# Optimization experiments

Hardware: AMD Instinct MI355X
Metric: run time of the kernel (lower is better)

The kernel has to match this reference:

```python
import jax, jax.numpy as jnp
import numpy as np

DIM = 1024
HEADS = 16
HEAD_DIM = DIM // HEADS
MLP_HID = 4 * DIM
LN_EPS = 1e-5


def layer_norm(x, g, b):
    mu = jnp.mean(x, axis=-1, keepdims=True)
    var = jnp.mean((x - mu) ** 2, axis=-1, keepdims=True)
    return (x - mu) * jax.lax.rsqrt(var + LN_EPS) * g + b


def setup_inputs() -> dict:
    key = jax.random.key(0)
    ks = jax.random.split(key, 8)
    s = 0.02
    return {
        "x": jax.random.normal(ks[0], (8, 1024, DIM), dtype=jnp.float32),
        "attention_mask": jnp.ones((8, 1024), dtype=jnp.int32),
        "ln1_g": jnp.ones((DIM,), jnp.float32),
        "ln1_b": jnp.zeros((DIM,), jnp.float32),
        "qkv_w": jax.random.normal(ks[1], (3 * DIM, DIM), jnp.float32) * s,
        "proj_w": jax.random.normal(ks[2], (DIM, DIM), jnp.float32) * s,
        "proj_b": jnp.zeros((DIM,), jnp.float32),
        "ln2_g": jnp.ones((DIM,), jnp.float32),
        "ln2_b": jnp.zeros((DIM,), jnp.float32),
        "fc1_w": jax.random.normal(ks[3], (MLP_HID, DIM), jnp.float32) * s,
        "fc1_b": jnp.zeros((MLP_HID,), jnp.float32),
        "fc2_w": jax.random.normal(ks[4], (DIM, MLP_HID), jnp.float32) * s,
        "fc2_b": jnp.zeros((DIM,), jnp.float32),
    }


def reference(x, attention_mask, ln1_g, ln1_b, qkv_w, proj_w, proj_b,
              ln2_g, ln2_b, fc1_w, fc1_b, fc2_w, fc2_b):
    B, N, C = x.shape
    scale = HEAD_DIM ** -0.5

    # --- attention branch ---
    h = layer_norm(x, ln1_g, ln1_b)
    qkv = h @ qkv_w.T                       # [B,N,3C] (no qkv bias)
    qkv = qkv.reshape(B, N, 3, HEADS, HEAD_DIM).transpose(2, 0, 3, 1, 4)
    q, k, v = qkv[0], qkv[1], qkv[2]        # each [B,H,N,Dh]
    attn = jnp.einsum('bhnd,bhmd->bhnm', q, k) * scale
    mask = (attention_mask == 0)[:, None, None, :]  # [B,1,1,N]
    attn = jnp.where(mask, -jnp.inf, attn)
    attn = jax.nn.softmax(attn, axis=-1)
    out = jnp.einsum('bhnm,bhmd->bhnd', attn, v)
    out = out.transpose(0, 2, 1, 3).reshape(B, N, C)
    out = out @ proj_w.T + proj_b
    x = x + out

    # --- MLP branch ---
    h = layer_norm(x, ln2_g, ln2_b)
    h = jax.nn.gelu(h @ fc1_w.T + fc1_b, approximate=False)
    h = h @ fc2_w.T + fc2_b
    return x + h
```

## Files before the change

kernel.cpp:

```cpp
#include <hip/hip_runtime.h>
#include <hip/hip_bf16.h>
#include <stdint.h>
#include <math.h>

#define DIMC 1024
#define SEQ 1024
#define NBATCH 8
#define NHEADS 16
#define HDIM 64
#define MLPHID 4096
#define NROWS (NBATCH*SEQ)

typedef __attribute__((ext_vector_type(8))) short short8;
typedef __attribute__((ext_vector_type(4))) float f32x4;
typedef __attribute__((ext_vector_type(16))) float f32x16;
typedef __attribute__((ext_vector_type(4))) unsigned int u32x4;

__device__ __forceinline__ short f2bf(float f) {
  union { float f; uint32_t u; } x; x.f = f;
  uint32_t r = (x.u + 0x7FFFu + ((x.u >> 16) & 1u)) >> 16;
  return (short)r;
}

__device__ __forceinline__ unsigned int cvtpk(float lo, float hi_) {
  unsigned int r;
  asm("v_cvt_pk_bf16_f32 %0, %1, %2" : "=v"(r) : "v"(lo), "v"(hi_));
  return r;
}

__device__ __forceinline__ float gelu_f(float v) {
  const float t = v * v;
  const float p = fmaf(t, 0.044715f, 1.0f);
  const float e = __builtin_amdgcn_exp2f(2.3022082f * v * p);
  return v - v * __builtin_amdgcn_rcpf(e + 1.0f);
}

__device__ __forceinline__ f32x4 mfma16(short8 a, short8 b, f32x4 c) {
  return __builtin_amdgcn_mfma_f32_16x16x32_bf16(a, b, c, 0, 0, 0);
}
__device__ __forceinline__ f32x16 mfma32(short8 a, short8 b, f32x16 c) {
  return __builtin_amdgcn_mfma_f32_32x32x16_bf16(a, b, c, 0, 0, 0);
}

__device__ __forceinline__ void gload16(const void* g, void* l) {
  __builtin_amdgcn_global_load_lds(
      (const __attribute__((address_space(1))) uint32_t*)g,
      (__attribute__((address_space(3))) uint32_t*)l, 16, 0, 0);
}

__global__ __launch_bounds__(256)
void f2bw_kernel(const float* __restrict__ w0, const float* __restrict__ w1,
                 const float* __restrict__ w2, const float* __restrict__ w3,
                 short* __restrict__ o0, short* __restrict__ o1,
                 short* __restrict__ o2, short* __restrict__ o3) {
  const int i = blockIdx.x * 256 + threadIdx.x;
  const float4* src;
  short4* dst;
  if (i < 786432)       { src = (const float4*)w0 + i;             dst = (short4*)o0 + i; }
  else if (i < 1048576) { src = (const float4*)w1 + (i - 786432);  dst = (short4*)o1 + (i - 786432); }
  else if (i < 2097152) { src = (const float4*)w2 + (i - 1048576); dst = (short4*)o2 + (i - 1048576); }
  else                  { src = (const float4*)w3 + (i - 2097152); dst = (short4*)o3 + (i - 2097152); }
  const float4 v = *src;
  short4 o;
  o.x = f2bf(v.x); o.y = f2bf(v.y); o.z = f2bf(v.z); o.w = f2bf(v.w);
  *dst = o;
}

__global__ __launch_bounds__(256)
void ln_kernel(const float* __restrict__ x, const float* __restrict__ g,
               const float* __restrict__ beta, short* __restrict__ out) {
  const int row = blockIdx.x;
  const int tid = threadIdx.x;
  const float4 v = ((const float4*)(x + (size_t)row * DIMC))[tid];
  float s = v.x + v.y + v.z + v.w;
  float q = v.x*v.x + v.y*v.y + v.z*v.z + v.w*v.w;
#pragma unroll
  for (int o = 32; o > 0; o >>= 1) { s += __shfl_down(s, o); q += __shfl_down(q, o); }
  __shared__ float rs[4], rq[4];
  const int lane = tid & 63, w = tid >> 6;
  if (lane == 0) { rs[w] = s; rq[w] = q; }
  __syncthreads();
  s = rs[0] + rs[1] + rs[2] + rs[3];
  q = rq[0] + rq[1] + rq[2] + rq[3];
  const float mean = s * (1.0f / DIMC);
  const float var = q * (1.0f / DIMC) - mean * mean;
  const float rstd = rsqrtf(var + 1e-5f);
  const float4 gv = ((const float4*)g)[tid];
  const float4 bv = ((const float4*)beta)[tid];
  short4 o4;
  o4.x = f2bf((v.x - mean) * rstd * gv.x + bv.x);
  o4.y = f2bf((v.y - mean) * rstd * gv.y + bv.y);
  o4.z = f2bf((v.z - mean) * rstd * gv.z + bv.z);
  o4.w = f2bf((v.w - mean) * rstd * gv.w + bv.w);
  ((short4*)(out + (size_t)row * DIMC))[tid] = o4;
}

#define NOVM ((void)0)
#define NOST ((void)0)
#define VMC4 asm volatile("s_waitcnt vmcnt(4)" ::: "memory")
#define VMC2 asm volatile("s_waitcnt vmcnt(2)" ::: "memory")

#define SA(DB, H, T) \
  gload16(sA0 + (H)*hstep + (size_t)(T)*64, stb + ((DB)*4 + (H))*16384); \
  gload16(sA1 + (H)*hstep + (size_t)(T)*64, stb + ((DB)*4 + (H))*16384 + 8192)

#define SB(DB, H, T) \
  gload16(sB0 + (H)*hstep + (size_t)(T)*64, stb + ((DB)*4 + 2 + (H))*16384); \
  gload16(sB1 + (H)*hstep + (size_t)(T)*64, stb + ((DB)*4 + 2 + (H))*16384 + 8192)

#define PH(DB, QA, QB, LDA, LDB, STAGE, VM) \
  do { \
    if (LDA) { \
      _Pragma("unroll") \
      for (int mi = 0; mi < 4; ++mi) { \
        _Pragma("unroll") \
        for (int ks = 0; ks < 2; ++ks) \
          af[mi][ks] = *(const short8*)(ard##DB + (((QA)*4 + mi)*2 + ks)*1024); \
      } \
    } \
    if (LDB) { \
      _Pragma("unroll") \
      for (int ni = 0; ni < 2; ++ni) { \
        _Pragma("unroll") \
        for (int ks = 0; ks < 2; ++ks) \
          bfv[QB][ni][ks] = *(const short8*)(brd##DB + (((QB)*2 + ni)*2 + ks)*1024); \
      } \
    } \
    STAGE; \
    __builtin_amdgcn_s_barrier(); \
    asm volatile("s_waitcnt lgkmcnt(0)" ::: "memory"); \
    __builtin_amdgcn_sched_barrier(0); \
    __builtin_amdgcn_s_setprio(1); \
    _Pragma("unroll") \
    for (int ks = 0; ks < 2; ++ks) { \
      _Pragma("unroll") \
      for (int mi = 0; mi < 4; ++mi) { \
        _Pragma("unroll") \
        for (int ni = 0; ni < 2; ++ni) \
          acc[(QA)*4 + mi][(QB)*2 + ni] = \
            mfma16(af[mi][ks], bfv[QB][ni][ks], acc[(QA)*4 + mi][(QB)*2 + ni]); \
      } \
    } \
    __builtin_amdgcn_s_setprio(0); \
    VM; \
    __builtin_amdgcn_s_barrier(); \
  } while (0)

template<bool BIAS, bool GELU, bool RESID, bool OBF16>
__global__ __launch_bounds__(512)
void gemm8p(const short* __restrict__ A, const short* __restrict__ W,
            const float* __restrict__ bias, const float* __restrict__ resid,
            float* __restrict__ outF, short* __restrict__ outB,
            int M, int N, int K, int ntl, int mt8)
{
  __shared__ __align__(16) char lsm[131072];
  const int tid = threadIdx.x;
  const int lane = tid & 63;
  const int w = tid >> 6;
  const int wm = w >> 2;
  const int wn = w & 3;
  const int fr = lane & 15;
  const int fko = (lane >> 4) << 3;

  const int bid = blockIdx.x;
  const int xcd = bid & 7, l = bid >> 3;
  const int bm = (xcd * mt8 + l / ntl) << 8;
  const int bn = (l % ntl) << 8;

  int row_[2], kk_[2];
#pragma unroll
  for (int j = 0; j < 2; ++j) {
    const int s = j * 8 + (tid >> 6);
    const int r16 = (tid & 63) >> 2;
    const int cb = ((tid & 3) << 4) ^ (((tid >> 5) & 1) << 5);
    row_[j] = (s >> 1) * 16 + r16;
    kk_[j]  = (s & 1) * 32 + (cb >> 1);
  }
  const short* sA0 = A + (size_t)(bm + row_[0]) * K + kk_[0];
  const short* sA1 = A + (size_t)(bm + row_[1]) * K + kk_[1];
  const short* sB0 = W + (size_t)(bn + row_[0]) * K + kk_[0];
  const short* sB1 = W + (size_t)(bn + row_[1]) * K + kk_[1];
  const size_t hstep = (size_t)128 * K;
  char* stb = lsm + tid * 16;

  const int lofs = fr * 64 + ((fko << 1) ^ (((fr >> 3) & 1) << 5));
  const char* ard0 = lsm + wm * 16384 + lofs;
  const char* brd0 = lsm + 32768 + (wn >> 1) * 16384 + (wn & 1) * 8192 + lofs;
  const char* ard1 = ard0 + 65536;
  const char* brd1 = brd0 + 65536;

  short8 af[4][2];
  short8 bfv[2][2][2];
  f32x4 acc[8][4] = {};

  SA(0, 0, 0); SA(0, 1, 0);
  SB(0, 0, 0); SB(0, 1, 0);
  SB(1, 0, 1); SB(1, 1, 1);
  VMC4;
  __builtin_amdgcn_s_barrier();

  const int nk = K >> 6;
  const int nit = nk >> 1;
  const int tmask = nk - 1;
  for (int it = 0; it < nit; ++it) {
    const int t1 = 2 * it + 1;
    const int t2 = (2 * it + 2) & tmask;
    const int t3 = (2 * it + 3) & tmask;
    PH(0, 0, 0, 1, 1, SA(1, 0, t1), NOVM);
    PH(0, 0, 1, 0, 1, SA(1, 1, t1), NOVM);
    PH(0, 1, 1, 1, 0, SB(0, 0, t2), NOVM);
    PH(0, 1, 0, 0, 0, SB(0, 1, t2), VMC4);
    PH(1, 0, 0, 1, 1, SA(0, 0, t2), NOVM);
    PH(1, 0, 1, 0, 1, SA(0, 1, t2), NOVM);
    PH(1, 1, 1, 1, 0, SB(1, 0, t3), NOVM);
    PH(1, 1, 0, 0, 0, SB(1, 1, t3), VMC4);
  }

  asm volatile("s_waitcnt vmcnt(0)" ::: "memory");
  __builtin_amdgcn_s_barrier();

  const int orow0 = bm + wm * 128 + ((lane >> 4) << 2);
  const int ocol0 = bn + wn * 64 + fr;
#pragma unroll
  for (int mi = 0; mi < 8; ++mi) {
#pragma unroll
    for (int r = 0; r < 4; ++r) {
      const int row = orow0 + mi * 16 + r;
      const size_t base = (size_t)row * N;
#pragma unroll
      for (int ni = 0; ni < 4; ++ni) {
        const int col = ocol0 + ni * 16;
        float v = acc[mi][ni][r];
        if (BIAS) v += bias[col];
        if (GELU) v = gelu_f(v);
        if (RESID) v += resid[base + col];
        if (OBF16) outB[base + col] = f2bf(v);
        else       outF[base + col] = v;
      }
    }
  }
}

#define SA2(DB, H, T) \
  gload16(sA0 + (H)*hstep + (size_t)(T)*64, stb + ((DB)*3 + (H))*16384); \
  gload16(sA1 + (H)*hstep + (size_t)(T)*64, stb + ((DB)*3 + (H))*16384 + 8192)

#define SB2(DB, T) \
  gload16(sB0 + (size_t)(T)*64, stb + ((DB)*3 + 2)*16384); \
  gload16(sB1 + (size_t)(T)*64, stb + ((DB)*3 + 2)*16384 + 8192)

#define PH2(DB, QA, QB, LDA, LDB, STAGE, VM) \
  do { \
    if (LDA) { \
      _Pragma("unroll") \
      for (int i = 0; i < 2; ++i) { \
        _Pragma("unroll") \
        for (int ks = 0; ks < 2; ++ks) \
          af[i][ks] = *(const short8*)(ard##DB + (((QA)*2 + i)*2 + ks)*1024); \
      } \
    } \
    if (LDB) { \
      _Pragma("unroll") \
      for (int jn = 0; jn < 2; ++jn) { \
        _Pragma("unroll") \
        for (int ks = 0; ks < 2; ++ks) \
          bfv[QB][jn][ks] = *(const short8*)(brd##DB + (((QB)*2 + jn)*2 + ks)*1024); \
      } \
    } \
    STAGE; \
    __builtin_amdgcn_s_barrier(); \
    asm volatile("s_waitcnt lgkmcnt(0)" ::: "memory"); \
    __builtin_amdgcn_sched_barrier(0); \
    __builtin_amdgcn_s_setprio(1); \
    _Pragma("unroll") \
    for (int ks = 0; ks < 2; ++ks) { \
      _Pragma("unroll") \
      for (int i = 0; i < 2; ++i) { \
        _Pragma("unroll") \
        for (int jn = 0; jn < 2; ++jn) \
          acc[(QA)*2 + i][(QB)*2 + jn] = \
            mfma16(af[i][ks], bfv[QB][jn][ks], acc[(QA)*2 + i][(QB)*2 + jn]); \
      } \
    } \
    __builtin_amdgcn_s_setprio(0); \
    VM; \
    __builtin_amdgcn_s_barrier(); \
  } while (0)

template<bool BIAS, bool GELU, bool RESID, bool OBF16, bool QSCALE>
__global__ __launch_bounds__(512)
void gemm8pn(const short* __restrict__ A, const short* __restrict__ W,
             const float* __restrict__ bias, const float* __restrict__ resid,
             float* __restrict__ outF, short* __restrict__ outB,
             int M, int N, int K, int ntl, int mt8)
{
  __shared__ __align__(16) char lsm[98304];
  const int tid = threadIdx.x;
  const int lane = tid & 63;
  const int w = tid >> 6;
  const int wm = w >> 1;
  const int wn = w & 1;
  const int fr = lane & 15;
  const int fko = (lane >> 4) << 3;

  const int bid = blockIdx.x;
  const int xcd = bid & 7, l = bid >> 3;
  const int bm = (xcd * mt8 + l / ntl) << 8;
  const int bn = (l % ntl) << 7;

  int row_[2], kk_[2];
#pragma unroll
  for (int j = 0; j < 2; ++j) {
    const int s = j * 8 + (tid >> 6);
    const int r16 = (tid & 63) >> 2;
    const int cb = ((tid & 3) << 4) ^ (((tid >> 5) & 1) << 5);
    row_[j] = (s >> 1) * 16 + r16;
    kk_[j]  = (s & 1) * 32 + (cb >> 1);
  }
  const short* sA0 = A + (size_t)(bm + row_[0]) * K + kk_[0];
  const short* sA1 = A + (size_t)(bm + row_[1]) * K + kk_[1];
  const short* sB0 = W + (size_t)(bn + row_[0]) * K + kk_[0];
  const short* sB1 = W + (size_t)(bn + row_[1]) * K + kk_[1];
  const size_t hstep = (size_t)128 * K;
  char* stb = lsm + tid * 16;

  const int lofs = fr * 64 + ((fko << 1) ^ (((fr >> 3) & 1) << 5));
  const char* ard0 = lsm + (wm >> 1) * 16384 + (wm & 1) * 8192 + lofs;
  const char* brd0 = lsm + 32768 + wn * 8192 + lofs;
  const char* ard1 = ard0 + 49152;
  const char* brd1 = brd0 + 49152;

  short8 af[2][2];
  short8 bfv[2][2][2];
  f32x4 acc[4][4] = {};

  SA2(0, 0, 0); SA2(0, 1, 0); SB2(0, 0);
  SB2(1, 1);
  VMC2;
  __builtin_amdgcn_s_barrier();

  const int nk = K >> 6;
  const int nit = nk >> 1;
  const int tmask = nk - 1;
  for (int it = 0; it < nit; ++it) {
    const int t1 = 2 * it + 1;
    const int t2 = (2 * it + 2) & tmask;
    const int t3 = (2 * it + 3) & tmask;
    PH2(0, 0, 0, 1, 1, SA2(1, 0, t1), NOVM);
    PH2(0, 0, 1, 0, 1, SA2(1, 1, t1), NOVM);
    PH2(0, 1, 1, 1, 0, SB2(0, t2),    NOVM);
    PH2(0, 1, 0, 0, 0, NOST,          VMC2);
    PH2(1, 0, 0, 1, 1, SA2(0, 0, t2), NOVM);
    PH2(1, 0, 1, 0, 1, SA2(0, 1, t2), NOVM);
    PH2(1, 1, 1, 1, 0, SB2(1, t3),    NOVM);
    PH2(1, 1, 0, 0, 0, NOST,          VMC2);
  }

  asm volatile("s_waitcnt vmcnt(0)" ::: "memory");
  __builtin_amdgcn_s_barrier();

  const int orow0 = bm + wm * 64 + ((lane >> 4) << 2);
  const int ocol0 = bn + wn * 64 + fr;
#pragma unroll
  for (int mi = 0; mi < 4; ++mi) {
#pragma unroll
    for (int r = 0; r < 4; ++r) {
      const int row = orow0 + mi * 16 + r;
      const size_t base = (size_t)row * N;
#pragma unroll
      for (int ni = 0; ni < 4; ++ni) {
        const int col = ocol0 + ni * 16;
        float v = acc[mi][ni][r];
        if (BIAS) v += bias[col];
        if (GELU) v = gelu_f(v);
        if (QSCALE) v *= (col < 1024 ? 0.18033688f : 1.0f);
        if (RESID) v += resid[base + col];
        if (OBF16) outB[base + col] = f2bf(v);
        else       outF[base + col] = v;
      }
    }
  }
}

__global__ __launch_bounds__(256)
void attn_kernel(const short* __restrict__ qkv, const int* __restrict__ amask,
                 short* __restrict__ out)
{
  __shared__ __align__(16) char lsm[36864];
  char* lsK = lsm;
  char* lsV = lsm + 16384;
  int* lmask = (int*)(lsm + 32768);
  __shared__ int anym;

  const int tid = threadIdx.x;
  const int lane = tid & 63;
  const int w = tid >> 6;
  const int l31 = lane & 31;
  const int hi = lane >> 5;
  const int swz = (l31 & 7) << 4;

  const int bid = blockIdx.x;
  const int swzb = ((bid & 7) << 7) | (bid >> 3);
  const int qt = swzb & 7;
  const int h = (swzb >> 3) & 15;
  const int b = swzb >> 7;
  const size_t rowbase = (size_t)b * SEQ;
  const short* qkvB = qkv + rowbase * 3072 + h * 64;

  const int4 mv = ((const int4*)(amask + b * SEQ))[tid];
  if (tid == 0) anym = 0;
  ((int4*)lmask)[tid] = mv;
  __syncthreads();
  if ((mv.x & mv.y & mv.z & mv.w) == 0) atomicOr(&anym, 1);

  const int q0 = qt * 128 + w * 32;
  const short* qptr = qkvB + (size_t)(q0 + l31) * 3072;
  short8 qf[4];
#pragma unroll
  for (int ks = 0; ks < 4; ++ks)
    qf[ks] = *(const short8*)(qptr + ks * 16 + hi * 8);

  const int krow = tid >> 3;
  const int kcc = (((tid & 7) * 16) ^ ((krow & 7) << 4)) >> 1;
  const short* gK = qkvB + 1024 + kcc;
  char* ldK = lsK + tid * 16;
  const int vr = tid & 63;
  const int vc0 = (tid >> 6) << 3;
  const short* gV = qkvB + 2048 + vc0;

  gload16(gK + (size_t)krow * 3072, ldK);
  gload16(gK + (size_t)(krow + 32) * 3072, ldK + 4096);
  {
    short8 a0 = *(const short8*)(gV + (size_t)vr * 3072);
    short8 a1 = *(const short8*)(gV + (size_t)vr * 3072 + 32);
#pragma unroll
    for (int j = 0; j < 8; ++j) {
      *(short*)(lsV + (vc0 + j) * 128 + ((2 * vr) ^ (j << 4))) = a0[j];
      *(short*)(lsV + (vc0 + 32 + j) * 128 + ((2 * vr) ^ (j << 4))) = a1[j];
    }
  }
  __syncthreads();

  f32x16 oacc[2] = {};
  float psum = 0.f;

  for (int c = 0; c < 16; ++c) {
    const int cur = c & 1;
    const char* lKc = lsK + cur * 8192;
    const char* lVc = lsV + cur * 8192;
    const bool pf = (c < 15);
    short8 vv0, vv1;
    if (pf) {
      const size_t nb_ = (size_t)(c + 1) * 64;
      char* ldKn = ldK + (cur ^ 1) * 8192;
      gload16(gK + (nb_ + krow) * 3072, ldKn);
      gload16(gK + (nb_ + krow + 32) * 3072, ldKn + 4096);
      vv0 = *(const short8*)(gV + (nb_ + vr) * 3072);
      vv1 = *(const short8*)(gV + (nb_ + vr) * 3072 + 32);
    }

    f32x16 pacc[2] = {};
    __builtin_amdgcn_s_setprio(1);
#pragma unroll
    for (int ks = 0; ks < 4; ++ks) {
#pragma unroll
      for (int s = 0; s < 2; ++s) {
        short8 kf = *(const short8*)(lKc + (s * 32 + l31) * 128 +
                                     ((ks * 32 + hi * 16) ^ swz));
        pacc[s] = mfma32(kf, qf[ks], pacc[s]);
      }
    }
    __builtin_amdgcn_s_setprio(0);

    if (pf) {
      char* lVn = lsV + (cur ^ 1) * 8192;
#pragma unroll
      for (int j = 0; j < 8; ++j) {
        *(short*)(lVn + (vc0 + j) * 128 + ((2 * vr) ^ (j << 4))) = vv0[j];
        *(short*)(lVn + (vc0 + 32 + j) * 128 + ((2 * vr) ^ (j << 4))) = vv1[j];
      }
    }

    if (anym) {
      const int kv0 = c * 64;
#pragma unroll
      for (int s = 0; s < 2; ++s)
#pragma unroll
        for (int r = 0; r < 16; ++r) {
          const int kv = kv0 + 32 * s + (r & 3) + 8 * (r >> 2) + 4 * hi;
          if (lmask[kv] == 0) pacc[s][r] = -1e30f;
        }
    }

    float pe[2][16];
#pragma unroll
    for (int s = 0; s < 2; ++s)
#pragma unroll
      for (int r = 0; r < 16; ++r) {
        const float p = __builtin_amdgcn_exp2f(pacc[s][r]);
        pe[s][r] = p;
        psum += p;
      }

    short8 pa[4];
#pragma unroll
    for (int ks = 0; ks < 4; ++ks) {
      const int sh = ks >> 1, kb = (ks & 1) << 3;
      unsigned int aa = cvtpk(pe[sh][kb + 0], pe[sh][kb + 1]);
      unsigned int bb = cvtpk(pe[sh][kb + 4], pe[sh][kb + 5]);
      unsigned int cc = cvtpk(pe[sh][kb + 2], pe[sh][kb + 3]);
      unsigned int dd = cvtpk(pe[sh][kb + 6], pe[sh][kb + 7]);
      asm volatile("v_permlane32_swap_b32 %0, %1" : "+v"(aa), "+v"(bb));
      asm volatile("v_permlane32_swap_b32 %0, %1" : "+v"(cc), "+v"(dd));
      u32x4 t;
      t[0] = aa; t[1] = cc; t[2] = bb; t[3] = dd;
      pa[ks] = __builtin_bit_cast(short8, t);
    }

    __builtin_amdgcn_s_setprio(1);
#pragma unroll
    for (int nb = 0; nb < 2; ++nb)
#pragma unroll
      for (int ks = 0; ks < 4; ++ks) {
        short8 vf = *(const short8*)(lVc + (nb * 32 + l31) * 128 +
                                     ((ks * 32 + hi * 16) ^ swz));
        oacc[nb] = mfma32(pa[ks], vf, oacc[nb]);
      }
    __builtin_amdgcn_s_setprio(0);

    __syncthreads();
  }

  const float lt = psum + __shfl_xor(psum, 32);
  const size_t orow = rowbase + q0;
#pragma unroll
  for (int r = 0; r < 16; ++r) {
    const int q = (r & 3) + 8 * (r >> 2) + 4 * hi;
    const float linv = 1.0f / __shfl(lt, q);
    short* op = out + (orow + q) * DIMC + h * 64 + l31;
    op[0]  = f2bf(oacc[0][r] * linv);
    op[32] = f2bf(oacc[1][r] * linv);
  }
}

extern "C" void kernel_launch(void* const* d_in, const int* in_sizes, int n_in,
                              void* d_out, int out_size, void* d_ws, size_t ws_size,
                              hipStream_t stream)
{
  const float* x      = (const float*)d_in[0];
  const int*   amask  = (const int*)d_in[1];
  const float* ln1_g  = (const float*)d_in[2];
  const float* ln1_b  = (const float*)d_in[3];
  const float* qkv_w  = (const float*)d_in[4];
  const float* proj_w = (const float*)d_in[5];
  const float* proj_b = (const float*)d_in[6];
  const float* ln2_g  = (const float*)d_in[7];
  const float* ln2_b  = (const float*)d_in[8];
  const float* fc1_w  = (const float*)d_in[9];
  const float* fc1_b  = (const float*)d_in[10];
  const float* fc2_w  = (const float*)d_in[11];
  const float* fc2_b  = (const float*)d_in[12];
  float* out = (float*)d_out;

  char* ws = (char*)d_ws;
  short* wqkv  = (short*)(ws);
  short* wproj = (short*)(ws + 6291456);
  short* wfc1  = (short*)(ws + 8388608);
  short* wfc2  = (short*)(ws + 16777216);
  float* x1    = (float*)(ws + 25165824);
  short* hb    = (short*)(ws + 58720256);
  short* qkvo  = (short*)(ws + 75497472);
  short* attno = (short*)(ws + 125829120);
  short* fc1o  = (short*)(ws + 75497472);

  f2bw_kernel<<<12288, 256, 0, stream>>>(qkv_w, proj_w, fc1_w, fc2_w,
                                         wqkv, wproj, wfc1, wfc2);

  ln_kernel<<<NROWS, 256, 0, stream>>>(x, ln1_g, ln1_b, hb);

  gemm8pn<false, false, false, true, true><<<768, 512, 0, stream>>>(
      hb, wqkv, nullptr, nullptr, nullptr, qkvo, NROWS, 3 * DIMC, DIMC, 24, 4);

  attn_kernel<<<1024, 256, 0, stream>>>(qkvo, amask, attno);

  gemm8pn<true, false, true, false, false><<<256, 512, 0, stream>>>(
      attno, wproj, proj_b, x, x1, nullptr, NROWS, DIMC, DIMC, 8, 4);

  ln_kernel<<<NROWS, 256, 0, stream>>>(x1, ln2_g, ln2_b, hb);

  gemm8p<true, true, false, true><<<512, 512, 0, stream>>>(
      hb, wfc1, fc1_b, nullptr, nullptr, fc1o, NROWS, MLPHID, DIMC, 16, 4);

  gemm8pn<true, false, true, false, false><<<256, 512, 0, stream>>>(
      fc1o, wfc2, fc2_b, x1, out, nullptr, NROWS, DIMC, MLPHID, 8, 4);
}
```

Measured before the change: 327.1 us.

## Fuse weight cast with LN1, store residual in bf16, restructure narrow GEMM pipeline

Merges the weight fp32-to-bf16 conversion and the first layernorm into one launch. It also stores the intermediate residual x1 as bf16 instead of fp32, which roughly halves its write and read traffic in the projection GEMM, LN2 and the fc2 epilogue. The narrow GEMM is rewritten with a different k-step pipeline: a full A tile is double-buffered and B tiles rotate through three buffers in 112KB of LDS. Rounding x1 to bf16 before adding it back to the final residual lowers accuracy, and the larger LDS footprint may reduce occupancy.

```diff
diff --git a/kernel.cpp b/kernel.cpp
--- a/kernel.cpp
+++ b/kernel.cpp
@@ -22,6 +22,11 @@
   return (short)r;
 }
 
+__device__ __forceinline__ float bf2f(unsigned short b) {
+  union { uint32_t u; float f; } c; c.u = ((uint32_t)b) << 16;
+  return c.f;
+}
+
 __device__ __forceinline__ unsigned int cvtpk(float lo, float hi_) {
   unsigned int r;
   asm("v_cvt_pk_bf16_f32 %0, %1, %2" : "=v"(r) : "v"(lo), "v"(hi_));
@@ -49,29 +54,66 @@
 }
 
 __global__ __launch_bounds__(256)
-void f2bw_kernel(const float* __restrict__ w0, const float* __restrict__ w1,
+void prep_kernel(const float* __restrict__ x, const float* __restrict__ g,
+                 const float* __restrict__ beta, short* __restrict__ hb,
+                 const float* __restrict__ w0, const float* __restrict__ w1,
                  const float* __restrict__ w2, const float* __restrict__ w3,
                  short* __restrict__ o0, short* __restrict__ o1,
                  short* __restrict__ o2, short* __restrict__ o3) {
-  const int i = blockIdx.x * 256 + threadIdx.x;
-  const float4* src;
-  short4* dst;
-  if (i < 786432)       { src = (const float4*)w0 + i;             dst = (short4*)o0 + i; }
-  else if (i < 1048576) { src = (const float4*)w1 + (i - 786432);  dst = (short4*)o1 + (i - 786432); }
-  else if (i < 2097152) { src = (const float4*)w2 + (i - 1048576); dst = (short4*)o2 + (i - 1048576); }
-  else                  { src = (const float4*)w3 + (i - 2097152); dst = (short4*)o3 + (i - 2097152); }
-  const float4 v = *src;
-  short4 o;
-  o.x = f2bf(v.x); o.y = f2bf(v.y); o.z = f2bf(v.z); o.w = f2bf(v.w);
-  *dst = o;
-}
-
+  const int tid = threadIdx.x;
+  if (blockIdx.x < NROWS) {
+    const int row = blockIdx.x;
+    const float4 v = ((const float4*)(x + (size_t)row * DIMC))[tid];
+    float s = v.x + v.y + v.z + v.w;
+    float q = v.x*v.x + v.y*v.y + v.z*v.z + v.w*v.w;
+#pragma unroll
+    for (int o = 32; o > 0; o >>= 1) { s += __shfl_down(s, o); q += __shfl_down(q, o); }
+    __shared__ float rs[4], rq[4];
+    const int lane = tid & 63, w = tid >> 6;
+    if (lane == 0) { rs[w] = s; rq[w] = q; }
+    __syncthreads();
+    s = rs[0] + rs[1] + rs[2] + rs[3];
+    q = rq[0] + rq[1] + rq[2] + rq[3];
+    const float mean = s * (1.0f / DIMC);
+    const float var = q * (1.0f / DIMC) - mean * mean;
+    const float rstd = rsqrtf(var + 1e-5f);
+    const float4 gv = ((const float4*)g)[tid];
+    const float4 bv = ((const float4*)beta)[tid];
+    short4 o4;
+    o4.x = f2bf((v.x - mean) * rstd * gv.x + bv.x);
+    o4.y = f2bf((v.y - mean) * rstd * gv.y + bv.y);
+    o4.z = f2bf((v.z - mean) * rstd * gv.z + bv.z);
+    o4.w = f2bf((v.w - mean) * rstd * gv.w + bv.w);
+    ((short4*)(hb + (size_t)row * DIMC))[tid] = o4;
+  } else {
+    const int i = (blockIdx.x - NROWS) * 256 + tid;
+    const float4* src;
+    short4* dst;
+    if (i < 786432)       { src = (const float4*)w0 + i;             dst = (short4*)o0 + i; }
+    else if (i < 1048576) { src = (const float4*)w1 + (i - 786432);  dst = (short4*)o1 + (i - 786432); }
+    else if (i < 2097152) { src = (const float4*)w2 + (i - 1048576); dst = (short4*)o2 + (i - 1048576); }
+    else                  { src = (const float4*)w3 + (i - 2097152); dst = (short4*)o3 + (i - 2097152); }
+    const float4 v = *src;
+    short4 o;
+    o.x = f2bf(v.x); o.y = f2bf(v.y); o.z = f2bf(v.z); o.w = f2bf(v.w);
+    *dst = o;
+  }
+}
+
+template<bool INBF16>
 __global__ __launch_bounds__(256)
-void ln_kernel(const float* __restrict__ x, const float* __restrict__ g,
+void ln_kernel(const void* __restrict__ xin, const float* __restrict__ g,
                const float* __restrict__ beta, short* __restrict__ out) {
   const int row = blockIdx.x;
   const int tid = threadIdx.x;
-  const float4 v = ((const float4*)(x + (size_t)row * DIMC))[tid];
+  float4 v;
+  if (INBF16) {
+    const short4 vb = ((const short4*)xin)[row * 256 + tid];
+    v.x = bf2f((unsigned short)vb.x); v.y = bf2f((unsigned short)vb.y);
+    v.z = bf2f((unsigned short)vb.z); v.w = bf2f((unsigned short)vb.w);
+  } else {
+    v = ((const float4*)xin)[row * 256 + tid];
+  }
   float s = v.x + v.y + v.z + v.w;
   float q = v.x*v.x + v.y*v.y + v.z*v.z + v.w*v.w;
 #pragma unroll
@@ -94,6 +136,7 @@
   o4.w = f2bf((v.w - mean) * rstd * gv.w + bv.w);
   ((short4*)(out + (size_t)row * DIMC))[tid] = o4;
 }
+
 
 #define NOVM ((void)0)
 #define NOST ((void)0)
@@ -241,60 +284,48 @@
   }
 }
 
-#define SA2(DB, H, T) \
-  gload16(sA0 + (H)*hstep + (size_t)(T)*64, stb + ((DB)*3 + (H))*16384); \
-  gload16(sA1 + (H)*hstep + (size_t)(T)*64, stb + ((DB)*3 + (H))*16384 + 8192)
-
-#define SB2(DB, T) \
-  gload16(sB0 + (size_t)(T)*64, stb + ((DB)*3 + 2)*16384); \
-  gload16(sB1 + (size_t)(T)*64, stb + ((DB)*3 + 2)*16384 + 8192)
-
-#define PH2(DB, QA, QB, LDA, LDB, STAGE, VM) \
+#define SAK(SLOT, T) \
+  gload16(sA0 + (size_t)(T)*64,         (SLOT) + tid*16); \
+  gload16(sA1 + (size_t)(T)*64,         (SLOT) + 8192 + tid*16); \
+  gload16(sA0 + hstep + (size_t)(T)*64, (SLOT) + 16384 + tid*16); \
+  gload16(sA1 + hstep + (size_t)(T)*64, (SLOT) + 24576 + tid*16)
+
+#define SBK(SLOT, T) \
+  gload16(sB0 + (size_t)(T)*64, (SLOT) + tid*16); \
+  gload16(sB1 + (size_t)(T)*64, (SLOT) + 8192 + tid*16)
+
+#define PHK(ARD, BRD, KS, STAGE, VM) \
   do { \
-    if (LDA) { \
-      _Pragma("unroll") \
-      for (int i = 0; i < 2; ++i) { \
-        _Pragma("unroll") \
-        for (int ks = 0; ks < 2; ++ks) \
-          af[i][ks] = *(const short8*)(ard##DB + (((QA)*2 + i)*2 + ks)*1024); \
-      } \
-    } \
-    if (LDB) { \
-      _Pragma("unroll") \
-      for (int jn = 0; jn < 2; ++jn) { \
-        _Pragma("unroll") \
-        for (int ks = 0; ks < 2; ++ks) \
-          bfv[QB][jn][ks] = *(const short8*)(brd##DB + (((QB)*2 + jn)*2 + ks)*1024); \
-      } \
-    } \
+    _Pragma("unroll") \
+    for (int mi = 0; mi < 4; ++mi) \
+      af[mi] = *(const short8*)((ARD) + (mi*2 + (KS))*1024); \
+    _Pragma("unroll") \
+    for (int jn = 0; jn < 4; ++jn) \
+      bfq[jn] = *(const short8*)((BRD) + (jn*2 + (KS))*1024); \
     STAGE; \
     __builtin_amdgcn_s_barrier(); \
     asm volatile("s_waitcnt lgkmcnt(0)" ::: "memory"); \
     __builtin_amdgcn_sched_barrier(0); \
     __builtin_amdgcn_s_setprio(1); \
     _Pragma("unroll") \
-    for (int ks = 0; ks < 2; ++ks) { \
+    for (int mi = 0; mi < 4; ++mi) { \
       _Pragma("unroll") \
-      for (int i = 0; i < 2; ++i) { \
-        _Pragma("unroll") \
-        for (int jn = 0; jn < 2; ++jn) \
-          acc[(QA)*2 + i][(QB)*2 + jn] = \
-            mfma16(af[i][ks], bfv[QB][jn][ks], acc[(QA)*2 + i][(QB)*2 + jn]); \
-      } \
+      for (int jn = 0; jn < 4; ++jn) \
+        acc[mi][jn] = mfma16(af[mi], bfq[jn], acc[mi][jn]); \
     } \
     __builtin_amdgcn_s_setprio(0); \
     VM; \
     __builtin_amdgcn_s_barrier(); \
   } while (0)
 
-template<bool BIAS, bool GELU, bool RESID, bool OBF16, bool QSCALE>
+template<bool BIAS, bool GELU, bool RESID, bool RESB16, bool OBF16, bool QSCALE>
 __global__ __launch_bounds__(512)
-void gemm8pn(const short* __restrict__ A, const short* __restrict__ W,
-             const float* __restrict__ bias, const float* __restrict__ resid,
-             float* __restrict__ outF, short* __restrict__ outB,
-             int M, int N, int K, int ntl, int mt8)
+void gemm2k(const short* __restrict__ A, const short* __restrict__ W,
+            const float* __restrict__ bias, const void* __restrict__ resid,
+            float* __restrict__ outF, short* __restrict__ outB,
+            int M, int N, int K, int ntl, int mt8)
 {
-  __shared__ __align__(16) char lsm[98304];
+  __shared__ __align__(16) char lsm[114688];
   const int tid = threadIdx.x;
   const int lane = tid & 63;
   const int w = tid >> 6;
@@ -322,38 +353,45 @@
   const short* sB0 = W + (size_t)(bn + row_[0]) * K + kk_[0];
   const short* sB1 = W + (size_t)(bn + row_[1]) * K + kk_[1];
   const size_t hstep = (size_t)128 * K;
-  char* stb = lsm + tid * 16;
 
   const int lofs = fr * 64 + ((fko << 1) ^ (((fr >> 3) & 1) << 5));
-  const char* ard0 = lsm + (wm >> 1) * 16384 + (wm & 1) * 8192 + lofs;
-  const char* brd0 = lsm + 32768 + wn * 8192 + lofs;
-  const char* ard1 = ard0 + 49152;
-  const char* brd1 = brd0 + 49152;
-
-  short8 af[2][2];
-  short8 bfv[2][2][2];
+  const char* ard0 = lsm + wm * 8192 + lofs;
+  const char* ard1 = ard0 + 32768;
+  char* as0 = lsm;
+  char* as1 = lsm + 32768;
+  const char* bur = lsm + 65536 + 0 * 16384 + wn * 8192 + lofs;
+  const char* bvr = lsm + 65536 + 1 * 16384 + wn * 8192 + lofs;
+  const char* bwr = lsm + 65536 + 2 * 16384 + wn * 8192 + lofs;
+  char* bus = lsm + 65536 + 0 * 16384;
+  char* bvs = lsm + 65536 + 1 * 16384;
+  char* bws = lsm + 65536 + 2 * 16384;
+
+  short8 af[4];
+  short8 bfq[4];
   f32x4 acc[4][4] = {};
-
-  SA2(0, 0, 0); SA2(0, 1, 0); SB2(0, 0);
-  SB2(1, 1);
-  VMC2;
-  __builtin_amdgcn_s_barrier();
 
   const int nk = K >> 6;
   const int nit = nk >> 1;
   const int tmask = nk - 1;
+
+  SAK(as0, 0);
+  SBK(bus, 0);
+  SBK(bvs, 1);
+  asm volatile("s_waitcnt vmcnt(0)" ::: "memory");
+  __builtin_amdgcn_s_barrier();
+
   for (int it = 0; it < nit; ++it) {
-    const int t1 = 2 * it + 1;
+    const int v  = 2 * it + 1;
     const int t2 = (2 * it + 2) & tmask;
     const int t3 = (2 * it + 3) & tmask;
-    PH2(0, 0, 0, 1, 1, SA2(1, 0, t1), NOVM);
-    PH2(0, 0, 1, 0, 1, SA2(1, 1, t1), NOVM);
-    PH2(0, 1, 1, 1, 0, SB2(0, t2),    NOVM);
-    PH2(0, 1, 0, 0, 0, NOST,          VMC2);
-    PH2(1, 0, 0, 1, 1, SA2(0, 0, t2), NOVM);
-    PH2(1, 0, 1, 0, 1, SA2(0, 1, t2), NOVM);
-    PH2(1, 1, 1, 1, 0, SB2(1, t3),    NOVM);
-    PH2(1, 1, 0, 0, 0, NOST,          VMC2);
+    PHK(ard0, bur, 0, SAK(as1, v),  NOVM);
+    PHK(ard0, bur, 1, SBK(bws, t2), VMC2);
+    PHK(ard1, bvr, 0, SAK(as0, t2), NOVM);
+    PHK(ard1, bvr, 1, SBK(bus, t3), VMC2);
+    const char* tr;
+    tr = bur; bur = bwr; bwr = bvr; bvr = tr;
+    char* ts;
+    ts = bus; bus = bws; bws = bvs; bvs = ts;
   }
 
   asm volatile("s_waitcnt vmcnt(0)" ::: "memory");
@@ -374,7 +412,10 @@
         if (BIAS) v += bias[col];
         if (GELU) v = gelu_f(v);
         if (QSCALE) v *= (col < 1024 ? 0.18033688f : 1.0f);
-        if (RESID) v += resid[base + col];
+        if (RESID) {
+          if (RESB16) v += bf2f(((const unsigned short*)resid)[base + col]);
+          else        v += ((const float*)resid)[base + col];
+        }
         if (OBF16) outB[base + col] = f2bf(v);
         else       outF[base + col] = v;
       }
@@ -567,30 +608,29 @@
   short* wproj = (short*)(ws + 6291456);
   short* wfc1  = (short*)(ws + 8388608);
   short* wfc2  = (short*)(ws + 16777216);
-  float* x1    = (float*)(ws + 25165824);
+  short* x1b   = (short*)(ws + 25165824);
   short* hb    = (short*)(ws + 58720256);
   short* qkvo  = (short*)(ws + 75497472);
   short* attno = (short*)(ws + 125829120);
   short* fc1o  = (short*)(ws + 75497472);
 
-  f2bw_kernel<<<12288, 256, 0, stream>>>(qkv_w, proj_w, fc1_w, fc2_w,
-                                         wqkv, wproj, wfc1, wfc2);
-
-  ln_kernel<<<NROWS, 256, 0, stream>>>(x, ln1_g, ln1_b, hb);
-
-  gemm8pn<false, false, false, true, true><<<768, 512, 0, stream>>>(
+  prep_kernel<<<NROWS + 12288, 256, 0, stream>>>(
+      x, ln1_g, ln1_b, hb, qkv_w, proj_w, fc1_w, fc2_w,
+      wqkv, wproj, wfc1, wfc2);
+
+  gemm2k<false, false, false, false, true, true><<<768, 512, 0, stream>>>(
       hb, wqkv, nullptr, nullptr, nullptr, qkvo, NROWS, 3 * DIMC, DIMC, 24, 4);
 
   attn_kernel<<<1024, 256, 0, stream>>>(qkvo, amask, attno);
 
-  gemm8pn<true, false, true, false, false><<<256, 512, 0, stream>>>(
-      attno, wproj, proj_b, x, x1, nullptr, NROWS, DIMC, DIMC, 8, 4);
-
-  ln_kernel<<<NROWS, 256, 0, stream>>>(x1, ln2_g, ln2_b, hb);
+  gemm2k<true, false, true, false, true, false><<<256, 512, 0, stream>>>(
+      attno, wproj, proj_b, x, nullptr, x1b, NROWS, DIMC, DIMC, 8, 4);
+
+  ln_kernel<true><<<NROWS, 256, 0, stream>>>(x1b, ln2_g, ln2_b, hb);
 
   gemm8p<true, true, false, true><<<512, 512, 0, stream>>>(
       hb, wfc1, fc1_b, nullptr, nullptr, fc1o, NROWS, MLPHID, DIMC, 16, 4);
 
-  gemm8pn<true, false, true, false, false><<<256, 512, 0, stream>>>(
-      fc1o, wfc2, fc2_b, x1, out, nullptr, NROWS, DIMC, MLPHID, 8, 4);
-}
+  gemm2k<true, false, true, true, false, false><<<256, 512, 0, stream>>>(
+      fc1o, wfc2, fc2_b, x1b, out, nullptr, NROWS, DIMC, MLPHID, 8, 4);
+}
```

Result: no change. 325.0 us (-0.7%).
